# Kernel optimization log

Measured on AMD Instinct MI355X. Metric: run time of the kernel, lower is better.

Reference implementation:

```python
import jax, jax.numpy as jnp
import numpy as np

B, NB, DIM, R = 4096, 64, 512, 4
INTER = DIM // R
EPS = 1e-5


def setup_inputs() -> dict:
    key = jax.random.key(0)
    ks = jax.random.split(key, 14)
    inp = {
        "t": jax.random.normal(ks[0], (B, NB, DIM), dtype=jnp.float32),
        # branch 1: Conv1d(dim->inter, k=1) == per-branch linear
        "W1": jax.random.normal(ks[1], (NB, INTER, DIM), dtype=jnp.float32) * 0.02,
        "b1": jax.random.normal(ks[2], (NB, INTER), dtype=jnp.float32) * 0.02,
        "g1": 1.0 + 0.1 * jax.random.normal(ks[3], (NB, INTER), dtype=jnp.float32),
        "beta1": 0.1 * jax.random.normal(ks[4], (NB, INTER), dtype=jnp.float32),
        "m1": 0.1 * jax.random.normal(ks[5], (NB, INTER), dtype=jnp.float32),
        "v1": jax.random.uniform(ks[6], (NB, INTER), dtype=jnp.float32, minval=0.5, maxval=1.5),
        # branch 2: Conv1d(inter->dim, k=1)
        "W2": jax.random.normal(ks[7], (NB, DIM, INTER), dtype=jnp.float32) * 0.02,
        "b2": jax.random.normal(ks[8], (NB, DIM), dtype=jnp.float32) * 0.02,
        "g2": 1.0 + 0.1 * jax.random.normal(ks[9], (NB, DIM), dtype=jnp.float32),
        "beta2": 0.1 * jax.random.normal(ks[10], (NB, DIM), dtype=jnp.float32),
        "m2": 0.1 * jax.random.normal(ks[11], (NB, DIM), dtype=jnp.float32),
        "v2": jax.random.uniform(ks[12], (NB, DIM), dtype=jnp.float32, minval=0.5, maxval=1.5),
    }
    return inp


def reference(t, W1, b1, g1, beta1, m1, v1, W2, b2, g2, beta2, m2, v2):
    # t: (B, nb, dim). torch: t.transpose(1,2).sum(-1) -> sum over nb axis.
    s = t.sum(axis=1)  # (B, dim)
    # All nb branches batched as one grouped GEMM: h = relu(BN1(W1 @ s + b1))
    h = jnp.einsum('nid,bd->bni', W1, s) + b1  # (B, nb, inter)
    h = (h - m1) * jax.lax.rsqrt(v1 + EPS) * g1 + beta1
    h = jax.nn.relu(h)
    y = jnp.einsum('ndi,bni->bnd', W2, h) + b2  # (B, nb, dim)
    y = (y - m2) * jax.lax.rsqrt(v2 + EPS) * g2 + beta2
    w = jax.nn.sigmoid(y)  # (B, nb, dim)
    # r = sum_j w[:, j, :] * t[:, j, :] * 3
    return (w * t).sum(axis=1) * 3.0  # (B, dim)
```

## Files before the change

### kernel.cpp

```cpp
#include <hip/hip_runtime.h>

#define B_SZ  4096
#define NB    64
#define DIM   512
#define INTER 128
#define EPSV  1e-5f

using f32x4  = __attribute__((ext_vector_type(4))) float;
using bf16x8 = __attribute__((ext_vector_type(8))) __bf16;
using short8 = __attribute__((ext_vector_type(8))) short;

static __device__ __forceinline__ unsigned short f2bf(float f) {
    union { float f; unsigned u; } v; v.f = f;
    return (unsigned short)((v.u + 0x7fffu + ((v.u >> 16) & 1u)) >> 16);
}

static __device__ __forceinline__ f32x4 mfma16(short8 a, short8 b, f32x4 c) {
    return __builtin_amdgcn_mfma_f32_16x16x32_bf16(
        __builtin_bit_cast(bf16x8, a), __builtin_bit_cast(bf16x8, b), c, 0, 0, 0);
}

__global__ void prep_kernel(
    const float4* __restrict__ W1, const float4* __restrict__ W2,
    const float* __restrict__ b1, const float* __restrict__ g1,
    const float* __restrict__ beta1, const float* __restrict__ m1,
    const float* __restrict__ v1,
    const float* __restrict__ b2, const float* __restrict__ g2,
    const float* __restrict__ beta2, const float* __restrict__ m2,
    const float* __restrict__ v2,
    ushort4* __restrict__ w1bf, ushort4* __restrict__ w2bf,
    float* __restrict__ sc1, float* __restrict__ bi1,
    float* __restrict__ sc2, float* __restrict__ bi2)
{
    int idx = blockIdx.x * blockDim.x + threadIdx.x;
    float4 a = W1[idx];
    ushort4 pa; pa.x = f2bf(a.x); pa.y = f2bf(a.y); pa.z = f2bf(a.z); pa.w = f2bf(a.w);
    w1bf[idx] = pa;
    float4 b = W2[idx];
    ushort4 pb; pb.x = f2bf(b.x); pb.y = f2bf(b.y); pb.z = f2bf(b.z); pb.w = f2bf(b.w);
    w2bf[idx] = pb;
    if (idx < NB * INTER) {
        float s = g1[idx] * rsqrtf(v1[idx] + EPSV);
        sc1[idx] = s;
        bi1[idx] = (b1[idx] - m1[idx]) * s + beta1[idx];
    }
    if (idx < NB * DIM) {
        float s = g2[idx] * rsqrtf(v2[idx] + EPSV);
        sc2[idx] = s;
        bi2[idx] = (b2[idx] - m2[idx]) * s + beta2[idx];
    }
}

__global__ void sum_kernel(const float* __restrict__ t, unsigned short* __restrict__ sbf)
{
    int tid = threadIdx.x;
    int b = blockIdx.x * 2 + (tid >> 7);
    int c = tid & 127;
    const float4* tb = (const float4*)t + (size_t)b * (NB * DIM / 4) + c;
    float4 acc = tb[0];
    for (int n = 1; n < NB; ++n) {
        float4 v = tb[n * (DIM / 4)];
        acc.x += v.x; acc.y += v.y; acc.z += v.z; acc.w += v.w;
    }
    ushort4 o; o.x = f2bf(acc.x); o.y = f2bf(acc.y); o.z = f2bf(acc.z); o.w = f2bf(acc.w);
    ((ushort4*)sbf)[(size_t)b * 128 + c] = o;
}

__global__ void zero_kernel(float4* __restrict__ out)
{
    out[blockIdx.x * 256 + threadIdx.x] = (float4){0.f, 0.f, 0.f, 0.f};
}

__global__ __launch_bounds__(256) void gemm1_kernel(
    const unsigned short* __restrict__ sbf,
    const unsigned short* __restrict__ w1bf,
    const float* __restrict__ sc1, const float* __restrict__ bi1,
    unsigned short* __restrict__ h)
{
    const int btile = blockIdx.x;
    const int n     = blockIdx.y;
    const int tid  = threadIdx.x;
    const int w    = tid >> 6;
    const int lane = tid & 63;
    const int quad = lane >> 4;
    const int l16  = lane & 15;
    const int m0 = btile * 128 + (w & 1) * 64;
    const int i0 = (w >> 1) * 64;

    f32x4 acc[4][4];
    #pragma unroll
    for (int a = 0; a < 4; ++a)
        #pragma unroll
        for (int c = 0; c < 4; ++c) acc[a][c] = (f32x4){0.f, 0.f, 0.f, 0.f};

    const unsigned short* w1n = w1bf + (size_t)n * (INTER * DIM);
    const unsigned short* abase = sbf + (size_t)(m0 + l16) * DIM + (quad << 3);
    const unsigned short* bbase = w1n + (size_t)(i0 + l16) * DIM + (quad << 3);

    #pragma unroll 2
    for (int s = 0; s < 16; ++s) {
        short8 af[4], bf[4];
        #pragma unroll
        for (int a = 0; a < 4; ++a)
            af[a] = *(const short8*)(abase + (size_t)(a * 16) * DIM + s * 32);
        #pragma unroll
        for (int c = 0; c < 4; ++c)
            bf[c] = *(const short8*)(bbase + (size_t)(c * 16) * DIM + s * 32);
        #pragma unroll
        for (int a = 0; a < 4; ++a)
            #pragma unroll
            for (int c = 0; c < 4; ++c)
                acc[a][c] = mfma16(af[a], bf[c], acc[a][c]);
    }

    unsigned short* hn = h + (size_t)n * (B_SZ * INTER);
    #pragma unroll
    for (int c = 0; c < 4; ++c) {
        const int i = i0 + c * 16 + l16;
        const float sc = sc1[n * INTER + i];
        const float bi = bi1[n * INTER + i];
        #pragma unroll
        for (int a = 0; a < 4; ++a) {
            #pragma unroll
            for (int r = 0; r < 4; ++r) {
                const int m = m0 + a * 16 + quad * 4 + r;
                float v = acc[a][c][r] * sc + bi;
                v = v > 0.f ? v : 0.f;
                hn[(size_t)m * INTER + i] = f2bf(v);
            }
        }
    }
}

__global__ __launch_bounds__(256) void gemm2_kernel(
    const float* __restrict__ t,
    const unsigned short* __restrict__ h,
    const unsigned short* __restrict__ w2bf,
    const float* __restrict__ sc2, const float* __restrict__ bi2,
    float* __restrict__ out)
{
    const int btile = blockIdx.x;
    const int dtile = blockIdx.y;
    const int ng    = blockIdx.z;
    const int tid  = threadIdx.x;
    const int w    = tid >> 6;
    const int lane = tid & 63;
    const int quad = lane >> 4;
    const int l16  = lane & 15;
    const int d0 = dtile * 64;

    f32x4 oacc[4];
    #pragma unroll
    for (int c = 0; c < 4; ++c) oacc[c] = (f32x4){0.f, 0.f, 0.f, 0.f};

    const unsigned short* habase =
        h + (size_t)(btile * 64 + w * 16 + l16) * INTER + (quad << 3);

    for (int n = ng * 32; n < ng * 32 + 32; ++n) {
        const unsigned short* hn  = habase + (size_t)n * (B_SZ * INTER);
        const unsigned short* w2n = w2bf + (size_t)n * (DIM * INTER)
                                  + (size_t)(d0 + l16) * INTER + (quad << 3);
        f32x4 yacc[4];
        #pragma unroll
        for (int c = 0; c < 4; ++c) yacc[c] = (f32x4){0.f, 0.f, 0.f, 0.f};

        #pragma unroll
        for (int s = 0; s < 4; ++s) {
            short8 af = *(const short8*)(hn + s * 32);
            #pragma unroll
            for (int c = 0; c < 4; ++c) {
                short8 bf = *(const short8*)(w2n + (size_t)(c * 16) * INTER + s * 32);
                yacc[c] = mfma16(af, bf, yacc[c]);
            }
        }

        #pragma unroll
        for (int c = 0; c < 4; ++c) {
            const int d = d0 + c * 16 + l16;
            const float sc = sc2[n * DIM + d];
            const float bi = bi2[n * DIM + d];
            #pragma unroll
            for (int r = 0; r < 4; ++r) {
                const int m = btile * 64 + w * 16 + quad * 4 + r;
                float y  = yacc[c][r] * sc + bi;
                float wv = 1.f / (1.f + __expf(-y));
                float tv = t[((size_t)m * NB + n) * DIM + d];
                oacc[c][r] += wv * tv;
            }
        }
    }

    #pragma unroll
    for (int c = 0; c < 4; ++c) {
        const int d = d0 + c * 16 + l16;
        #pragma unroll
        for (int r = 0; r < 4; ++r) {
            const int m = btile * 64 + w * 16 + quad * 4 + r;
            unsafeAtomicAdd(&out[(size_t)m * DIM + d], oacc[c][r] * 3.0f);
        }
    }
}

extern "C" void kernel_launch(void* const* d_in, const int* in_sizes, int n_in,
                              void* d_out, int out_size, void* d_ws, size_t ws_size,
                              hipStream_t stream)
{
    const float* t     = (const float*)d_in[0];
    const float* W1    = (const float*)d_in[1];
    const float* b1    = (const float*)d_in[2];
    const float* g1    = (const float*)d_in[3];
    const float* beta1 = (const float*)d_in[4];
    const float* m1    = (const float*)d_in[5];
    const float* v1    = (const float*)d_in[6];
    const float* W2    = (const float*)d_in[7];
    const float* b2    = (const float*)d_in[8];
    const float* g2    = (const float*)d_in[9];
    const float* beta2 = (const float*)d_in[10];
    const float* m2    = (const float*)d_in[11];
    const float* v2    = (const float*)d_in[12];

    char* ws = (char*)d_ws;
    unsigned short* w1bf = (unsigned short*)(ws);
    unsigned short* w2bf = (unsigned short*)(ws + 8388608);
    unsigned short* sbf  = (unsigned short*)(ws + 16777216);
    float* sc1 = (float*)(ws + 20971520);
    float* bi1 = (float*)(ws + 21004288);
    float* sc2 = (float*)(ws + 21037056);
    float* bi2 = (float*)(ws + 21168128);
    unsigned short* hbuf = (unsigned short*)(ws + 21299200);

    prep_kernel<<<4096, 256, 0, stream>>>(
        (const float4*)W1, (const float4*)W2,
        b1, g1, beta1, m1, v1, b2, g2, beta2, m2, v2,
        (ushort4*)w1bf, (ushort4*)w2bf, sc1, bi1, sc2, bi2);

    sum_kernel<<<2048, 256, 0, stream>>>(t, sbf);

    zero_kernel<<<2048, 256, 0, stream>>>((float4*)d_out);

    gemm1_kernel<<<dim3(32, 64), 256, 0, stream>>>(sbf, w1bf, sc1, bi1, hbuf);

    gemm2_kernel<<<dim3(64, 8, 2), 256, 0, stream>>>(t, hbuf, w2bf, sc2, bi2, (float*)d_out);
}
```

Before: 1.202 ms.

## Swap MFMA operand roles for vectorized stores and t loads, prefetch t, split more

```diff
diff --git a/kernel.cpp b/kernel.cpp
--- a/kernel.cpp
+++ b/kernel.cpp
@@ -5,6 +5,7 @@
 #define DIM   512
 #define INTER 128
 #define EPSV  1e-5f
+#define NLOG2E 1.4426950408889634f
 
 using f32x4  = __attribute__((ext_vector_type(4))) float;
 using bf16x8 = __attribute__((ext_vector_type(8))) __bf16;
@@ -46,8 +47,8 @@
     }
     if (idx < NB * DIM) {
         float s = g2[idx] * rsqrtf(v2[idx] + EPSV);
-        sc2[idx] = s;
-        bi2[idx] = (b2[idx] - m2[idx]) * s + beta2[idx];
+        sc2[idx] = -NLOG2E * s;
+        bi2[idx] = -NLOG2E * ((b2[idx] - m2[idx]) * s + beta2[idx]);
     }
 }
 
@@ -84,8 +85,8 @@
     const int lane = tid & 63;
     const int quad = lane >> 4;
     const int l16  = lane & 15;
-    const int m0 = btile * 128 + (w & 1) * 64;
-    const int i0 = (w >> 1) * 64;
+    const int i0 = (w & 1) * 64;
+    const int b0 = btile * 128 + (w >> 1) * 64;
 
     f32x4 acc[4][4];
     #pragma unroll
@@ -94,8 +95,8 @@
         for (int c = 0; c < 4; ++c) acc[a][c] = (f32x4){0.f, 0.f, 0.f, 0.f};
 
     const unsigned short* w1n = w1bf + (size_t)n * (INTER * DIM);
-    const unsigned short* abase = sbf + (size_t)(m0 + l16) * DIM + (quad << 3);
-    const unsigned short* bbase = w1n + (size_t)(i0 + l16) * DIM + (quad << 3);
+    const unsigned short* abase = w1n + (size_t)(i0 + l16) * DIM + (quad << 3);
+    const unsigned short* bbase = sbf + (size_t)(b0 + l16) * DIM + (quad << 3);
 
     #pragma unroll 2
     for (int s = 0; s < 16; ++s) {
@@ -115,19 +116,20 @@
 
     unsigned short* hn = h + (size_t)n * (B_SZ * INTER);
     #pragma unroll
-    for (int c = 0; c < 4; ++c) {
-        const int i = i0 + c * 16 + l16;
-        const float sc = sc1[n * INTER + i];
-        const float bi = bi1[n * INTER + i];
-        #pragma unroll
-        for (int a = 0; a < 4; ++a) {
-            #pragma unroll
-            for (int r = 0; r < 4; ++r) {
-                const int m = m0 + a * 16 + quad * 4 + r;
-                float v = acc[a][c][r] * sc + bi;
-                v = v > 0.f ? v : 0.f;
-                hn[(size_t)m * INTER + i] = f2bf(v);
-            }
+    for (int a = 0; a < 4; ++a) {
+        const int i = i0 + a * 16 + (quad << 2);
+        const f32x4 sv = *(const f32x4*)(sc1 + n * INTER + i);
+        const f32x4 bv = *(const f32x4*)(bi1 + n * INTER + i);
+        #pragma unroll
+        for (int c = 0; c < 4; ++c) {
+            const int b = b0 + c * 16 + l16;
+            ushort4 o;
+            float v0 = acc[a][c][0] * sv[0] + bv[0]; v0 = v0 > 0.f ? v0 : 0.f;
+            float v1 = acc[a][c][1] * sv[1] + bv[1]; v1 = v1 > 0.f ? v1 : 0.f;
+            float v2 = acc[a][c][2] * sv[2] + bv[2]; v2 = v2 > 0.f ? v2 : 0.f;
+            float v3 = acc[a][c][3] * sv[3] + bv[3]; v3 = v3 > 0.f ? v3 : 0.f;
+            o.x = f2bf(v0); o.y = f2bf(v1); o.z = f2bf(v2); o.w = f2bf(v3);
+            *(ushort4*)(hn + (size_t)b * INTER + i) = o;
         }
     }
 }
@@ -148,55 +150,69 @@
     const int quad = lane >> 4;
     const int l16  = lane & 15;
     const int d0 = dtile * 64;
+    const int b  = btile * 64 + w * 16 + l16;
+    const int dq = d0 + (quad << 2);
 
     f32x4 oacc[4];
     #pragma unroll
     for (int c = 0; c < 4; ++c) oacc[c] = (f32x4){0.f, 0.f, 0.f, 0.f};
 
-    const unsigned short* habase =
-        h + (size_t)(btile * 64 + w * 16 + l16) * INTER + (quad << 3);
-
-    for (int n = ng * 32; n < ng * 32 + 32; ++n) {
-        const unsigned short* hn  = habase + (size_t)n * (B_SZ * INTER);
-        const unsigned short* w2n = w2bf + (size_t)n * (DIM * INTER)
-                                  + (size_t)(d0 + l16) * INTER + (quad << 3);
+    const unsigned short* hb  = h + (size_t)(ng * 16) * (B_SZ * INTER)
+                              + (size_t)b * INTER + (quad << 3);
+    const unsigned short* w2b = w2bf + (size_t)(ng * 16) * (DIM * INTER)
+                              + (size_t)(d0 + l16) * INTER + (quad << 3);
+    const float* tb = t + ((size_t)b * NB + ng * 16) * DIM + dq;
+
+    f32x4 tc[4], tn[4];
+    #pragma unroll
+    for (int c = 0; c < 4; ++c) tc[c] = *(const f32x4*)(tb + c * 16);
+
+    for (int k = 0; k < 16; ++k) {
+        if (k < 15) {
+            const float* tnx = tb + (size_t)(k + 1) * DIM;
+            #pragma unroll
+            for (int c = 0; c < 4; ++c) tn[c] = *(const f32x4*)(tnx + c * 16);
+        }
+
+        const unsigned short* hn  = hb  + (size_t)k * (B_SZ * INTER);
+        const unsigned short* w2n = w2b + (size_t)k * (DIM * INTER);
         f32x4 yacc[4];
         #pragma unroll
         for (int c = 0; c < 4; ++c) yacc[c] = (f32x4){0.f, 0.f, 0.f, 0.f};
 
         #pragma unroll
         for (int s = 0; s < 4; ++s) {
-            short8 af = *(const short8*)(hn + s * 32);
+            short8 bfh = *(const short8*)(hn + s * 32);
             #pragma unroll
             for (int c = 0; c < 4; ++c) {
-                short8 bf = *(const short8*)(w2n + (size_t)(c * 16) * INTER + s * 32);
-                yacc[c] = mfma16(af, bf, yacc[c]);
+                short8 af = *(const short8*)(w2n + (size_t)(c * 16) * INTER + s * 32);
+                yacc[c] = mfma16(af, bfh, yacc[c]);
             }
         }
 
+        const int n = ng * 16 + k;
+        const float* scn = sc2 + (size_t)n * DIM + dq;
+        const float* bin = bi2 + (size_t)n * DIM + dq;
         #pragma unroll
         for (int c = 0; c < 4; ++c) {
-            const int d = d0 + c * 16 + l16;
-            const float sc = sc2[n * DIM + d];
-            const float bi = bi2[n * DIM + d];
+            const f32x4 sv = *(const f32x4*)(scn + c * 16);
+            const f32x4 bv = *(const f32x4*)(bin + c * 16);
             #pragma unroll
             for (int r = 0; r < 4; ++r) {
-                const int m = btile * 64 + w * 16 + quad * 4 + r;
-                float y  = yacc[c][r] * sc + bi;
-                float wv = 1.f / (1.f + __expf(-y));
-                float tv = t[((size_t)m * NB + n) * DIM + d];
-                oacc[c][r] += wv * tv;
+                float e  = yacc[c][r] * sv[r] + bv[r];
+                float wv = __builtin_amdgcn_rcpf(1.f + __builtin_amdgcn_exp2f(e));
+                oacc[c][r] += wv * tc[c][r];
             }
         }
+        #pragma unroll
+        for (int c = 0; c < 4; ++c) tc[c] = tn[c];
     }
 
     #pragma unroll
     for (int c = 0; c < 4; ++c) {
-        const int d = d0 + c * 16 + l16;
         #pragma unroll
         for (int r = 0; r < 4; ++r) {
-            const int m = btile * 64 + w * 16 + quad * 4 + r;
-            unsafeAtomicAdd(&out[(size_t)m * DIM + d], oacc[c][r] * 3.0f);
+            unsafeAtomicAdd(&out[(size_t)b * DIM + dq + c * 16 + r], oacc[c][r] * 3.0f);
         }
     }
 }
@@ -240,5 +256,5 @@
 
     gemm1_kernel<<<dim3(32, 64), 256, 0, stream>>>(sbf, w1bf, sc1, bi1, hbuf);
 
-    gemm2_kernel<<<dim3(64, 8, 2), 256, 0, stream>>>(t, hbuf, w2bf, sc2, bi2, (float*)d_out);
-}
+    gemm2_kernel<<<dim3(64, 8, 4), 256, 0, stream>>>(t, hbuf, w2bf, sc2, bi2, (float*)d_out);
+}
```

Measured after the change: 1.273 ms. 5.9% more time.
